# Performance work log

Measured on AMD Instinct MI355X. Metric: run time of the kernel, lower is better.

The kernel has to match this reference:

```python
import jax, jax.numpy as jnp
import numpy as np

B, T, K, D = 32, 512, 4, 256
E, M = 100000, 2048
NEG = -10000000000.0


def setup_inputs() -> dict:
    key = jax.random.key(0)
    ks = jax.random.split(key, 8)
    token_reprs = jax.random.normal(ks[0], (B, T, K, D), dtype=jnp.float32)
    edge_index = jax.random.randint(ks[1], (2, E), 0, B * T, dtype=jnp.int64)
    lm_indices = jax.random.randint(ks[2], (M,), 0, B * T * K, dtype=jnp.int64)
    batch_pointers = jax.random.randint(ks[3], (M,), 0, B, dtype=jnp.int64)
    tree_padding_mask = jax.random.bernoulli(ks[4], 0.8, (B, T))
    # SwiGLU(2*dim, 4*dim, 1) parameters (no biases)
    sg = 1.0 / np.sqrt(2 * D)
    sh = 1.0 / np.sqrt(4 * D)
    Wg = jax.random.normal(ks[5], (2 * D, 4 * D), dtype=jnp.float32) * sg
    Wv = jax.random.normal(ks[6], (2 * D, 4 * D), dtype=jnp.float32) * sg
    Wo = jax.random.normal(ks[7], (4 * D, 1), dtype=jnp.float32) * sh
    return {
        "token_reprs": token_reprs,
        "Wg": Wg,
        "Wv": Wv,
        "Wo": Wo,
        "edge_index": edge_index,
        "lm_indices": lm_indices,
        "batch_pointers": batch_pointers,
        "tree_padding_mask": tree_padding_mask,
    }


def reference(token_reprs, Wg, Wv, Wo, edge_index, lm_indices, batch_pointers, tree_padding_mask):
    b, t, k, d = token_reprs.shape
    # predict_lemmas: gather type reprs via edge_index, concat, SwiGLU MLP
    type_flat = token_reprs[:, :, 0].reshape(b * t, d)           # [B*T, D]
    scope_ids, goal_ids = edge_index[0], edge_index[1]
    x = jnp.concatenate([type_flat[scope_ids], type_flat[goal_ids]], axis=-1)  # [E, 2D]
    h = jax.nn.silu(x @ Wg) * (x @ Wv)                           # [E, 4D]
    lemmas = (h @ Wo).squeeze(-1)                                # [E]
    # predict_masks: gathers + masked dot-product scoring
    mask_reprs = token_reprs.reshape(-1, d)[lm_indices]          # [M, D]
    type_reprs = token_reprs[:, :, 0]                            # [B, T, D]
    candidates = type_reprs[batch_pointers]                      # [M, T, D]
    candidate_mask = tree_padding_mask[batch_pointers]           # [M, T]
    lm_preds = jnp.einsum('md,mtd->mt', mask_reprs, candidates)  # [M, T]
    lm_preds = jnp.where(candidate_mask, lm_preds, NEG)
    return lemmas, lm_preds
```

## Files before the change

kernel.cpp:

```cpp
#include <hip/hip_runtime.h>
#include <hip/hip_bf16.h>

typedef __bf16 bf16x8 __attribute__((ext_vector_type(8)));
typedef int   i32x8 __attribute__((ext_vector_type(8)));
typedef float f32x4 __attribute__((ext_vector_type(4)));

#define KDIM 512
#define NDIM 1024
#define DDIM 256
#define TDIM 512
#define MDIM 2048
#define NROWS 16384
#define NEGV -1e10f
#define NLM 128
#define WARR 524288

__device__ __forceinline__ unsigned int pk8(float a, float b, float c, float d) {
    unsigned int p = (unsigned int)__builtin_amdgcn_cvt_pk_fp8_f32(a, b, 0, 0);
    return (unsigned int)__builtin_amdgcn_cvt_pk_fp8_f32(c, d, (int)p, 1);
}

typedef const __attribute__((address_space(1))) unsigned int* gas_p;
typedef __attribute__((address_space(3))) unsigned int* las_p;
__device__ __forceinline__ void gl2lds16(const void* g, void* l) {
    __builtin_amdgcn_global_load_lds((gas_p)g, (las_p)l, 16, 0, 0);
}

__global__ void prep_all(const float* __restrict__ tok,
                         const float* __restrict__ Wg,
                         const float* __restrict__ Wv,
                         const int* __restrict__ bp,
                         unsigned char* __restrict__ tf8,
                         unsigned char* __restrict__ wp8,
                         int* __restrict__ counts,
                         unsigned short* __restrict__ lists) {
    const int bid = blockIdx.x;
    const int tid = threadIdx.x;
    if (bid == 0) {
        __shared__ int c[32];
        if (tid < 32) c[tid] = 0;
        __syncthreads();
        for (int m = tid; m < MDIM; m += 256) {
            int b = bp[m];
            int pos = atomicAdd(&c[b], 1);
            lists[b * MDIM + pos] = (unsigned short)m;
        }
        __syncthreads();
        if (tid < 32) counts[tid] = c[tid];
    } else if (bid <= 512) {
        __shared__ float tg[32][33];
        __shared__ float tv[32][33];
        int pb = bid - 1;
        int n0 = (pb & 31) * 32, k0 = (pb >> 5) * 32;
        {
            int kk = tid >> 3, nn = (tid & 7) * 4;
            float4 g = *(const float4*)(Wg + (size_t)(k0 + kk) * NDIM + n0 + nn);
            float4 v = *(const float4*)(Wv + (size_t)(k0 + kk) * NDIM + n0 + nn);
            tg[kk][nn] = g.x; tg[kk][nn + 1] = g.y; tg[kk][nn + 2] = g.z; tg[kk][nn + 3] = g.w;
            tv[kk][nn] = v.x; tv[kk][nn + 1] = v.y; tv[kk][nn + 2] = v.z; tv[kk][nn + 3] = v.w;
        }
        __syncthreads();
        int nn2 = tid >> 3, kk2 = (tid & 7) * 4;
        unsigned int pg = pk8(tg[kk2][nn2], tg[kk2 + 1][nn2],
                              tg[kk2 + 2][nn2], tg[kk2 + 3][nn2]);
        unsigned int pv = pk8(tv[kk2][nn2], tv[kk2 + 1][nn2],
                              tv[kk2 + 2][nn2], tv[kk2 + 3][nn2]);
        int n = n0 + nn2, k = k0 + kk2;
        int nt = n >> 6, wn = (n >> 5) & 1, ni = (n >> 4) & 1, cp = n & 15;
        int kc = k >> 7, rem = k & 127, qq = rem >> 5, hh = (rem >> 4) & 1, bb = rem & 15;
        int frag = ((nt * 4 + kc) * 2 + wn) * 2 + ni;
        size_t off = (size_t)frag * 2048 + (qq * 16 + cp) * 32 + hh * 16 + bb;
        *(unsigned int*)(wp8 + off) = pg;
        *(unsigned int*)(wp8 + WARR + off) = pv;
    } else {
        int g = ((bid - 513) * 256 + tid) * 16;
        int i = g >> 8, c = g & 255;
        const float* src = tok + (size_t)i * 1024 + c;
        unsigned int d[4];
#pragma unroll
        for (int j = 0; j < 4; j++) {
            float4 v = *(const float4*)(src + j * 4);
            d[j] = pk8(v.x, v.y, v.z, v.w);
        }
        uint4 o; o.x = d[0]; o.y = d[1]; o.z = d[2]; o.w = d[3];
        *(uint4*)(tf8 + g) = o;
    }
}

__launch_bounds__(256, 2)
__global__ void fused_main(const unsigned char* __restrict__ tf8,
                           const unsigned char* __restrict__ wp8,
                           const float* __restrict__ Wo,
                           const int* __restrict__ scope,
                           const int* __restrict__ goal,
                           float* __restrict__ outLem, int E,
                           const float* __restrict__ tok,
                           const int* __restrict__ lmi,
                           const int* __restrict__ counts,
                           const unsigned short* __restrict__ lists,
                           const int* __restrict__ tpm,
                           float* __restrict__ outP) {
    __shared__ unsigned char sA[64 * 1024];
    __shared__ float sRed[256];

    const int tid = threadIdx.x;
    const int lane = tid & 63;
    const int w = tid >> 6;
    const int col = lane & 15;
    const int q = lane >> 4;

    if ((int)blockIdx.x < NLM) {
        const int lb = blockIdx.x;
        const int b = lb & 31;
        const int t0 = (lb >> 5) * 128;
        const int cnt = counts[b];
        for (int mt = w * 16; mt < cnt; mt += 64) {
            int mc = mt + col;
            int aid = lists[b * MDIM + (mc < cnt ? mc : cnt - 1)];
            const float* arow = tok + (size_t)lmi[aid] * DDIM;
            i32x8 af[2];
#pragma unroll
            for (int kc = 0; kc < 2; kc++) {
                unsigned int d[8];
#pragma unroll
                for (int j = 0; j < 8; j++) {
                    float4 v = *(const float4*)(arow + kc * 128 + q * 32 + j * 4);
                    d[j] = pk8(v.x, v.y, v.z, v.w);
                }
                af[kc] = (i32x8){(int)d[0], (int)d[1], (int)d[2], (int)d[3],
                                 (int)d[4], (int)d[5], (int)d[6], (int)d[7]};
            }
            int gm[4];
#pragma unroll
            for (int r = 0; r < 4; r++) {
                int mrow = mt + q * 4 + r;
                gm[r] = (mrow < cnt) ? (int)lists[b * MDIM + mrow] : -1;
            }
#pragma unroll
            for (int ntile = 0; ntile < 8; ntile++) {
                int t = t0 + ntile * 16 + col;
                const unsigned char* brow = tf8 + (size_t)(b * TDIM + t) * DDIM;
                f32x4 acc = (f32x4){0.f, 0.f, 0.f, 0.f};
#pragma unroll
                for (int kc = 0; kc < 2; kc++) {
                    uint4 lo = *(const uint4*)(brow + kc * 128 + q * 32);
                    uint4 hi = *(const uint4*)(brow + kc * 128 + q * 32 + 16);
                    i32x8 bf = (i32x8){(int)lo.x, (int)lo.y, (int)lo.z, (int)lo.w,
                                       (int)hi.x, (int)hi.y, (int)hi.z, (int)hi.w};
                    acc = __builtin_amdgcn_mfma_scale_f32_16x16x128_f8f6f4(
                        af[kc], bf, acc, 0, 0, 0, 0x7F7F7F7F, 0, 0x7F7F7F7F);
                }
                int pmv = tpm[b * TDIM + t];
#pragma unroll
                for (int r = 0; r < 4; r++) {
                    if (gm[r] >= 0)
                        outP[(size_t)gm[r] * TDIM + t] = pmv ? acc[r] : NEGV;
                }
            }
        }
        return;
    }

    const int bx = blockIdx.x - NLM;
    const int etile = bx * 128;
    const int wm = w & 1;
    const int wn = w >> 1;

#pragma unroll
    for (int i = 0; i < 16; i++) {
        int r = w * 16 + i;
        int j = r & 1, kc = (r >> 1) & 3, mi = (r >> 3) & 3, am = r >> 5;
        int row = am * 64 + mi * 16 + col;
        int e = etile + row;
        int id = (e < E) ? ((kc < 2) ? scope[e] : goal[e]) : 0;
        gl2lds16(tf8 + (size_t)id * DDIM + (kc & 1) * 128 + q * 32 + j * 16,
                 &sA[r * 1024]);
    }
    __syncthreads();

    float lem[16];
#pragma unroll
    for (int i = 0; i < 16; i++) lem[i] = 0.f;

    const unsigned char* wbase = wp8 + lane * 32;

#define LOADB(s, buf)                                                          \
    {                                                                          \
        _Pragma("unroll")                                                      \
        for (int ni_ = 0; ni_ < 2; ni_++) {                                    \
            size_t f_ = (size_t)(((s) * 2 + wn) * 2 + ni_) * 2048;             \
            uint4 lo_ = *(const uint4*)(wbase + f_);                           \
            uint4 hi_ = *(const uint4*)(wbase + f_ + 16);                      \
            bgb[buf][ni_] = (i32x8){(int)lo_.x, (int)lo_.y, (int)lo_.z,        \
                (int)lo_.w, (int)hi_.x, (int)hi_.y, (int)hi_.z, (int)hi_.w};   \
            lo_ = *(const uint4*)(wbase + WARR + f_);                          \
            hi_ = *(const uint4*)(wbase + WARR + f_ + 16);                     \
            bvb[buf][ni_] = (i32x8){(int)lo_.x, (int)lo_.y, (int)lo_.z,        \
                (int)lo_.w, (int)hi_.x, (int)hi_.y, (int)hi_.z, (int)hi_.w};   \
        }                                                                      \
    }

    i32x8 bgb[2][2], bvb[2][2];
    LOADB(0, 0)

    for (int nt = 0; nt < 16; nt++) {
        f32x4 accG[4][2], accV[4][2];
#pragma unroll
        for (int mi = 0; mi < 4; mi++)
#pragma unroll
            for (int ni = 0; ni < 2; ni++) {
                accG[mi][ni] = (f32x4){0.f, 0.f, 0.f, 0.f};
                accV[mi][ni] = (f32x4){0.f, 0.f, 0.f, 0.f};
            }
#pragma unroll
        for (int kc = 0; kc < 4; kc++) {
            const int cur = kc & 1, nxt = cur ^ 1;
            LOADB(nt * 4 + kc + 1, nxt)
#pragma unroll
            for (int mi = 0; mi < 4; mi++) {
                int rb = ((wm * 4 + mi) * 4 + kc) * 2;
                uint4 lo = *(const uint4*)(&sA[rb * 1024 + lane * 16]);
                uint4 hi = *(const uint4*)(&sA[(rb + 1) * 1024 + lane * 16]);
                i32x8 af = (i32x8){(int)lo.x, (int)lo.y, (int)lo.z, (int)lo.w,
                                   (int)hi.x, (int)hi.y, (int)hi.z, (int)hi.w};
#pragma unroll
                for (int ni = 0; ni < 2; ni++) {
                    accG[mi][ni] = __builtin_amdgcn_mfma_scale_f32_16x16x128_f8f6f4(
                        af, bgb[cur][ni], accG[mi][ni], 0, 0, 0,
                        0x7F7F7F7F, 0, 0x7F7F7F7F);
                    accV[mi][ni] = __builtin_amdgcn_mfma_scale_f32_16x16x128_f8f6f4(
                        af, bvb[cur][ni], accV[mi][ni], 0, 0, 0,
                        0x7F7F7F7F, 0, 0x7F7F7F7F);
                }
            }
        }
#pragma unroll
        for (int ni = 0; ni < 2; ni++) {
            float wo = Wo[nt * 64 + wn * 32 + ni * 16 + col];
#pragma unroll
            for (int mi = 0; mi < 4; mi++)
#pragma unroll
                for (int r = 0; r < 4; r++) {
                    float g = accG[mi][ni][r];
                    float v = accV[mi][ni][r];
                    float s = g * __builtin_amdgcn_rcpf(1.f + __expf(-g));
                    lem[mi * 4 + r] += s * v * wo;
                }
        }
    }
#pragma unroll
    for (int i = 0; i < 16; i++) {
        float v = lem[i];
        for (int off = 8; off > 0; off >>= 1) v += __shfl_xor(v, off, 16);
        if (col == 0) {
            int row = wm * 64 + (i >> 2) * 16 + q * 4 + (i & 3);
            sRed[wn * 128 + row] = v;
        }
    }
    __syncthreads();
    if (tid < 128) {
        int e = etile + tid;
        if (e < E) outLem[e] = sRed[tid] + sRed[128 + tid];
    }
}

extern "C" void kernel_launch(void* const* d_in, const int* in_sizes, int n_in,
                              void* d_out, int out_size, void* d_ws, size_t ws_size,
                              hipStream_t stream) {
    const float* tok = (const float*)d_in[0];
    const float* Wg  = (const float*)d_in[1];
    const float* Wv  = (const float*)d_in[2];
    const float* Wo  = (const float*)d_in[3];
    const int* edge = (const int*)d_in[4];
    const int* lmi  = (const int*)d_in[5];
    const int* bp   = (const int*)d_in[6];
    const int* tpm  = (const int*)d_in[7];
    const int E = in_sizes[4] / 2;
    float* out = (float*)d_out;

    unsigned char* tf8 = (unsigned char*)d_ws;
    unsigned char* wp8 = tf8 + (size_t)NROWS * DDIM;
    int* counts = (int*)(wp8 + 2 * WARR);
    unsigned short* lists = (unsigned short*)(counts + 32);

    prep_all<<<dim3(1537), dim3(256), 0, stream>>>(
        tok, Wg, Wv, bp, tf8, wp8, counts, lists);
    int nLemBlocks = (E + 127) / 128;
    fused_main<<<dim3(NLM + nLemBlocks), dim3(256), 0, stream>>>(
        tf8, wp8, Wo, edge, edge + E, out, E,
        tok, lmi, counts, lists, tpm, out + E);
}
```

Before: 229.4 us.

## Switch lemma GEMM from 16x16x128 to 32x32x64 FP8 scaled MFMA

Result: slower. 279.4 us (+21.8%).

```diff
diff --git a/kernel.cpp b/kernel.cpp
--- a/kernel.cpp
+++ b/kernel.cpp
@@ -2,8 +2,9 @@
 #include <hip/hip_bf16.h>
 
 typedef __bf16 bf16x8 __attribute__((ext_vector_type(8)));
-typedef int   i32x8 __attribute__((ext_vector_type(8)));
-typedef float f32x4 __attribute__((ext_vector_type(4)));
+typedef int   i32x8  __attribute__((ext_vector_type(8)));
+typedef float f32x4  __attribute__((ext_vector_type(4)));
+typedef float f32x16 __attribute__((ext_vector_type(16)));
 
 #define KDIM 512
 #define NDIM 1024
@@ -65,11 +66,11 @@
                               tg[kk2 + 2][nn2], tg[kk2 + 3][nn2]);
         unsigned int pv = pk8(tv[kk2][nn2], tv[kk2 + 1][nn2],
                               tv[kk2 + 2][nn2], tv[kk2 + 3][nn2]);
-        int n = n0 + nn2, k = k0 + kk2;
-        int nt = n >> 6, wn = (n >> 5) & 1, ni = (n >> 4) & 1, cp = n & 15;
-        int kc = k >> 7, rem = k & 127, qq = rem >> 5, hh = (rem >> 4) & 1, bb = rem & 15;
-        int frag = ((nt * 4 + kc) * 2 + wn) * 2 + ni;
-        size_t off = (size_t)frag * 2048 + (qq * 16 + cp) * 32 + hh * 16 + bb;
+        int n32 = pb & 31;
+        int k64 = pb >> 6;
+        int khalf = (pb >> 5) & 1;
+        size_t off = (size_t)(n32 * 8 + k64) * 2048
+                   + (size_t)(khalf * 32 + nn2) * 32 + kk2;
         *(unsigned int*)(wp8 + off) = pg;
         *(unsigned int*)(wp8 + WARR + off) = pv;
     } else {
@@ -108,6 +109,8 @@
     const int w = tid >> 6;
     const int col = lane & 15;
     const int q = lane >> 4;
+    const int ln32 = lane & 31;
+    const int q2 = lane >> 5;
 
     if ((int)blockIdx.x < NLM) {
         const int lb = blockIdx.x;
@@ -168,34 +171,37 @@
 
 #pragma unroll
     for (int i = 0; i < 16; i++) {
-        int r = w * 16 + i;
-        int j = r & 1, kc = (r >> 1) & 3, mi = (r >> 3) & 3, am = r >> 5;
-        int row = am * 64 + mi * 16 + col;
+        int rc = w * 16 + i;
+        int j = rc & 1;
+        int reg = rc >> 1;
+        int g = reg >> 3, k64 = reg & 7;
+        int row = g * 32 + ln32;
         int e = etile + row;
-        int id = (e < E) ? ((kc < 2) ? scope[e] : goal[e]) : 0;
-        gl2lds16(tf8 + (size_t)id * DDIM + (kc & 1) * 128 + q * 32 + j * 16,
-                 &sA[r * 1024]);
+        int id = (e < E) ? ((k64 < 4) ? scope[e] : goal[e]) : 0;
+        gl2lds16(tf8 + (size_t)id * DDIM + (k64 & 3) * 64 + q2 * 32 + j * 16,
+                 &sA[reg * 2048 + j * 1024]);
     }
     __syncthreads();
 
-    float lem[16];
-#pragma unroll
-    for (int i = 0; i < 16; i++) lem[i] = 0.f;
+    float lem[32];
+#pragma unroll
+    for (int i = 0; i < 32; i++) lem[i] = 0.f;
 
     const unsigned char* wbase = wp8 + lane * 32;
 
 #define LOADB(s, buf)                                                          \
     {                                                                          \
         _Pragma("unroll")                                                      \
-        for (int ni_ = 0; ni_ < 2; ni_++) {                                    \
-            size_t f_ = (size_t)(((s) * 2 + wn) * 2 + ni_) * 2048;             \
+        for (int kk_ = 0; kk_ < 2; kk_++) {                                    \
+            size_t f_ = (size_t)((((s) >> 2) * 16) + wn * 8 +                  \
+                                 (((s) & 3) * 2) + kk_) * 2048;                \
             uint4 lo_ = *(const uint4*)(wbase + f_);                           \
             uint4 hi_ = *(const uint4*)(wbase + f_ + 16);                      \
-            bgb[buf][ni_] = (i32x8){(int)lo_.x, (int)lo_.y, (int)lo_.z,        \
+            bgb[buf][kk_] = (i32x8){(int)lo_.x, (int)lo_.y, (int)lo_.z,        \
                 (int)lo_.w, (int)hi_.x, (int)hi_.y, (int)hi_.z, (int)hi_.w};   \
             lo_ = *(const uint4*)(wbase + WARR + f_);                          \
             hi_ = *(const uint4*)(wbase + WARR + f_ + 16);                     \
-            bvb[buf][ni_] = (i32x8){(int)lo_.x, (int)lo_.y, (int)lo_.z,        \
+            bvb[buf][kk_] = (i32x8){(int)lo_.x, (int)lo_.y, (int)lo_.z,        \
                 (int)lo_.w, (int)hi_.x, (int)hi_.y, (int)hi_.z, (int)hi_.w};   \
         }                                                                      \
     }
@@ -204,57 +210,55 @@
     LOADB(0, 0)
 
     for (int nt = 0; nt < 16; nt++) {
-        f32x4 accG[4][2], accV[4][2];
-#pragma unroll
-        for (int mi = 0; mi < 4; mi++)
-#pragma unroll
-            for (int ni = 0; ni < 2; ni++) {
-                accG[mi][ni] = (f32x4){0.f, 0.f, 0.f, 0.f};
-                accV[mi][ni] = (f32x4){0.f, 0.f, 0.f, 0.f};
+        f32x16 accG[2], accV[2];
+#pragma unroll
+        for (int mi = 0; mi < 2; mi++)
+#pragma unroll
+            for (int r = 0; r < 16; r++) {
+                accG[mi][r] = 0.f;
+                accV[mi][r] = 0.f;
             }
 #pragma unroll
         for (int kc = 0; kc < 4; kc++) {
             const int cur = kc & 1, nxt = cur ^ 1;
             LOADB(nt * 4 + kc + 1, nxt)
 #pragma unroll
-            for (int mi = 0; mi < 4; mi++) {
-                int rb = ((wm * 4 + mi) * 4 + kc) * 2;
-                uint4 lo = *(const uint4*)(&sA[rb * 1024 + lane * 16]);
-                uint4 hi = *(const uint4*)(&sA[(rb + 1) * 1024 + lane * 16]);
-                i32x8 af = (i32x8){(int)lo.x, (int)lo.y, (int)lo.z, (int)lo.w,
-                                   (int)hi.x, (int)hi.y, (int)hi.z, (int)hi.w};
-#pragma unroll
-                for (int ni = 0; ni < 2; ni++) {
-                    accG[mi][ni] = __builtin_amdgcn_mfma_scale_f32_16x16x128_f8f6f4(
-                        af, bgb[cur][ni], accG[mi][ni], 0, 0, 0,
+            for (int mi = 0; mi < 2; mi++) {
+                int rbase = (wm * 2 + mi) * 8 + kc * 2;
+#pragma unroll
+                for (int kk = 0; kk < 2; kk++) {
+                    uint4 lo = *(const uint4*)(&sA[(rbase + kk) * 2048 + lane * 16]);
+                    uint4 hi = *(const uint4*)(&sA[(rbase + kk) * 2048 + 1024 + lane * 16]);
+                    i32x8 af = (i32x8){(int)lo.x, (int)lo.y, (int)lo.z, (int)lo.w,
+                                       (int)hi.x, (int)hi.y, (int)hi.z, (int)hi.w};
+                    accG[mi] = __builtin_amdgcn_mfma_scale_f32_32x32x64_f8f6f4(
+                        af, bgb[cur][kk], accG[mi], 0, 0, 0,
                         0x7F7F7F7F, 0, 0x7F7F7F7F);
-                    accV[mi][ni] = __builtin_amdgcn_mfma_scale_f32_16x16x128_f8f6f4(
-                        af, bvb[cur][ni], accV[mi][ni], 0, 0, 0,
+                    accV[mi] = __builtin_amdgcn_mfma_scale_f32_32x32x64_f8f6f4(
+                        af, bvb[cur][kk], accV[mi], 0, 0, 0,
                         0x7F7F7F7F, 0, 0x7F7F7F7F);
                 }
             }
         }
-#pragma unroll
-        for (int ni = 0; ni < 2; ni++) {
-            float wo = Wo[nt * 64 + wn * 32 + ni * 16 + col];
-#pragma unroll
-            for (int mi = 0; mi < 4; mi++)
-#pragma unroll
-                for (int r = 0; r < 4; r++) {
-                    float g = accG[mi][ni][r];
-                    float v = accV[mi][ni][r];
-                    float s = g * __builtin_amdgcn_rcpf(1.f + __expf(-g));
-                    lem[mi * 4 + r] += s * v * wo;
-                }
-        }
-    }
-#pragma unroll
-    for (int i = 0; i < 16; i++) {
+        float wo = Wo[nt * 64 + wn * 32 + ln32];
+#pragma unroll
+        for (int mi = 0; mi < 2; mi++)
+#pragma unroll
+            for (int r = 0; r < 16; r++) {
+                float g = accG[mi][r];
+                float v = accV[mi][r];
+                float s = g * __builtin_amdgcn_rcpf(1.f + __expf(-g));
+                lem[mi * 16 + r] += s * v * wo;
+            }
+    }
+#pragma unroll
+    for (int i = 0; i < 32; i++) {
         float v = lem[i];
-        for (int off = 8; off > 0; off >>= 1) v += __shfl_xor(v, off, 16);
-        if (col == 0) {
-            int row = wm * 64 + (i >> 2) * 16 + q * 4 + (i & 3);
-            sRed[wn * 128 + row] = v;
+        for (int off = 16; off > 0; off >>= 1) v += __shfl_xor(v, off, 32);
+        if (ln32 == 0) {
+            int mi = i >> 4, r = i & 15;
+            int row_local = (r & 3) + 8 * (r >> 2) + 4 * q2;
+            sRed[wn * 128 + wm * 64 + mi * 32 + row_local] = v;
         }
     }
     __syncthreads();
```
